# Kernel optimization log

Hardware: AMD Instinct MI355X
Metric: run time of the kernel (lower is better)

## Reference

```python
import jax, jax.numpy as jnp
import numpy as np

S = 41          # seq_len
D_IN = 1280
D_OUT = 1024
HEADS = 4
HC = D_OUT // HEADS
EPS = 1e-5

# ---- static edge construction (faithful to the torch code, incl. duplicate edges) ----

def _local_edges(s, window=1):
    e = []
    for i in range(s):
        for j in range(max(0, i - window), min(s, i + window + 1)):
            if i != j:
                e += [(i, j), (j, i)]
    return np.array(e, dtype=np.int32).T

def _region_edges(s):
    e = []
    step = s // 3
    for st in range(0, s, step):
        blk = range(st, min(st + step, s))
        for i in blk:
            for j in blk:
                if i != j:
                    e += [(i, j), (j, i)]
    return np.array(e, dtype=np.int32).T

def _global_edges(s):
    r, c = np.triu_indices(s, 1)  # torch.combinations: (i, j) with i < j
    return np.stack([r, c]).astype(np.int32)

def _batch_edges(e, b, s):
    off = np.arange(b, dtype=np.int32) * s
    return (e[:, None, :] + off[None, :, None]).reshape(2, -1)

_LOCAL = _local_edges(S)
_REGION = _region_edges(S)
_GLOBAL = _global_edges(S)

# ---- layer primitives ----

def _layernorm(x, g, b):
    mu = x.mean(-1, keepdims=True)
    v = ((x - mu) ** 2).mean(-1, keepdims=True)
    return (x - mu) / jnp.sqrt(v + EPS) * g + b

def _gcn(x, w, b, src, tgt, n):
    # PyG GCNConv: x' = D^-1/2 (A + I) D^-1/2 (x W) + b
    h = x @ w
    sl = jnp.arange(n, dtype=src.dtype)
    s = jnp.concatenate([src, sl]); t = jnp.concatenate([tgt, sl])
    deg = jax.ops.segment_sum(jnp.ones(t.shape, h.dtype), t, n)
    dinv = jnp.where(deg > 0, jax.lax.rsqrt(jnp.maximum(deg, 1.0)), 0.0)
    norm = dinv[s] * dinv[t]
    return jax.ops.segment_sum(h[s] * norm[:, None], t, n) + b

def _gat(x, w, a_src, a_dst, b, src, tgt, n):
    # PyG GATConv (shared lin, self loops, leaky_relu 0.2, softmax over incoming edges)
    h = (x @ w).reshape(n, HEADS, HC)
    sl = jnp.arange(n, dtype=src.dtype)
    s = jnp.concatenate([src, sl]); t = jnp.concatenate([tgt, sl])
    al_s = (h * a_src).sum(-1)  # [n, H]
    al_d = (h * a_dst).sum(-1)
    e = jax.nn.leaky_relu(al_s[s] + al_d[t], 0.2)  # [E, H]
    m = jax.ops.segment_max(e, t, n)
    ex = jnp.exp(e - m[t])
    den = jax.ops.segment_sum(ex, t, n)
    alpha = ex / den[t]
    out = jax.ops.segment_sum(h[s] * alpha[:, :, None], t, n)
    return out.reshape(n, HEADS * HC) + b

def _sage(x, wl, bl, wr, src, tgt, n):
    # PyG SAGEConv: mean-aggregate neighbors, plus root transform
    cnt = jax.ops.segment_sum(jnp.ones(src.shape, x.dtype), tgt, n)
    agg = jax.ops.segment_sum(x[src], tgt, n) / jnp.maximum(cnt, 1.0)[:, None]
    return agg @ wl + bl + x @ wr


def setup_inputs() -> dict:
    key = jax.random.key(0)
    ks = jax.random.split(key, 16)
    sc = 0.02
    f32 = jnp.float32
    inp = {
        'x': jax.random.normal(ks[0], (512, S, D_IN), f32),
        'att_w': jax.random.normal(ks[1], (D_IN, 1), f32) * sc,
        'att_b': jnp.zeros((1,), f32),
        'gcn_w': jax.random.normal(ks[2], (D_IN, D_OUT), f32) * sc,
        'gcn_b': jnp.zeros((D_OUT,), f32),
        'sn_g': jnp.ones((D_OUT,), f32), 'sn_b': jnp.zeros((D_OUT,), f32),
        'gat_w': jax.random.normal(ks[3], (D_IN, D_OUT), f32) * sc,
        'gat_as': jax.random.normal(ks[4], (HEADS, HC), f32) * sc,
        'gat_ad': jax.random.normal(ks[5], (HEADS, HC), f32) * sc,
        'gat_b': jnp.zeros((D_OUT,), f32),
        'mn_g': jnp.ones((D_OUT,), f32), 'mn_b': jnp.zeros((D_OUT,), f32),
        'sage_wl': jax.random.normal(ks[6], (D_IN, D_OUT), f32) * sc,
        'sage_bl': jnp.zeros((D_OUT,), f32),
        'sage_wr': jax.random.normal(ks[7], (D_IN, D_OUT), f32) * sc,
        'fp_w1': jax.random.normal(ks[8], (D_IN, 512), f32) * sc,
        'fp_b1': jnp.zeros((512,), f32),
        'fp_w2': jax.random.normal(ks[9], (512, S), f32) * sc,
        'fp_b2': jnp.zeros((S,), f32),
        'dn_g': jnp.ones((D_OUT,), f32), 'dn_b': jnp.zeros((D_OUT,), f32),
        'gate_w': jax.random.normal(ks[10], (3 * D_OUT, 3), f32) * sc,
        'gate_b': jnp.zeros((3,), f32),
    }
    return inp


def reference(x, att_w, att_b, gcn_w, gcn_b, sn_g, sn_b, gat_w, gat_as, gat_ad, gat_b,
              mn_g, mn_b, sage_wl, sage_bl, sage_wr, fp_w1, fp_b1, fp_w2, fp_b2,
              dn_g, dn_b, gate_w, gate_b):
    B = x.shape[0]
    N = B * S
    le = jnp.asarray(_batch_edges(_LOCAL, B, S))
    re = jnp.asarray(_batch_edges(_REGION, B, S))
    ge = jnp.asarray(_batch_edges(_GLOBAL, B, S))

    xf = x.reshape(N, D_IN)
    # shallow: local gating -> GCN -> LN
    enhanced = xf * jax.nn.sigmoid(xf @ att_w + att_b)
    shallow = _gcn(enhanced, gcn_w, gcn_b, le[0], le[1], N)
    shallow = _layernorm(shallow.reshape(B, S, D_OUT), sn_g, sn_b)
    # medium: GAT over region blocks -> LN
    gat = _gat(xf, gat_w, gat_as[None], gat_ad[None], gat_b, re[0], re[1], N)
    gat = _layernorm(gat.reshape(B, S, D_OUT), mn_g, mn_b)
    # deep: learned propagation mixing, SAGE over global edges -> LN
    pw = jax.nn.softmax(jax.nn.relu(x @ fp_w1 + fp_b1) @ fp_w2 + fp_b2, axis=-1)  # [B,S,S]
    sage_in = jnp.einsum('bij,bjd->bid', pw, x).reshape(N, D_IN)
    sage = _sage(sage_in, sage_wl, sage_bl, sage_wr, ge[0], ge[1], N)
    sage = _layernorm(sage.reshape(B, S, D_OUT), dn_g, dn_b)
    # gated branch mixing
    combined = jnp.concatenate([shallow, gat, sage], axis=-1)
    gates = jax.nn.softmax(combined @ gate_w + gate_b, axis=-1)
    total = gates[..., 0:1] * shallow + gates[..., 1:2] * gat + gates[..., 2:3] * sage
    return (shallow, gat, total)
```

## Files before the change

kernel.cpp:

```cpp
#include <hip/hip_runtime.h>
#include <math.h>

static constexpr int S    = 41;
static constexpr int DIN  = 1280;
static constexpr int DOUT = 1024;
static constexpr int HEADS = 4;
static constexpr int HC   = 256;

typedef __attribute__((ext_vector_type(4))) float f32x4;
typedef __attribute__((ext_vector_type(8))) short short8;

__device__ __forceinline__ ushort f2bf(float f) {
  uint u = __float_as_uint(f);
  uint r = u + 0x7fffu + ((u >> 16) & 1u);
  return (ushort)(r >> 16);
}
__device__ __forceinline__ float bf2f(ushort u) {
  return __uint_as_float(((uint)u) << 16);
}

__device__ __forceinline__ void gload16(const ushort* g, ushort* l) {
  __builtin_amdgcn_global_load_lds((const __attribute__((address_space(1))) void*)g,
                                   (__attribute__((address_space(3))) void*)l, 16, 0, 0);
}


__device__ __forceinline__ float warpReduceSum(float v) {
#pragma unroll
  for (int off = 32; off; off >>= 1) v += __shfl_down(v, off);
  return v;
}

__device__ __forceinline__ void blockReduce2(float& a, float& b) {
  a = warpReduceSum(a);
  b = warpReduceSum(b);
  __shared__ float red[8];
  int w = threadIdx.x >> 6, lane = threadIdx.x & 63;
  if (lane == 0) { red[w] = a; red[4 + w] = b; }
  __syncthreads();
  a = red[0] + red[1] + red[2] + red[3];
  b = red[4] + red[5] + red[6] + red[7];
}

__device__ __forceinline__ void blockReduce3(float& a, float& b, float& c) {
  a = warpReduceSum(a);
  b = warpReduceSum(b);
  c = warpReduceSum(c);
  __shared__ float red3[12];
  int w = threadIdx.x >> 6, lane = threadIdx.x & 63;
  if (lane == 0) { red3[w] = a; red3[4 + w] = b; red3[8 + w] = c; }
  __syncthreads();
  a = red3[0] + red3[1] + red3[2] + red3[3];
  b = red3[4] + red3[5] + red3[6] + red3[7];
  c = red3[8] + red3[9] + red3[10] + red3[11];
}


__global__ __launch_bounds__(256) void cvtsig_kernel(
    const float4* __restrict__ x, const float* __restrict__ att_w,
    const float* __restrict__ att_b, ushort4* __restrict__ xb, float* __restrict__ sig)
{
  int row  = blockIdx.x * 4 + (threadIdx.x >> 6);
  int lane = threadIdx.x & 63;
  const float4* xr = x + (size_t)row * (DIN / 4);
  const float4* wr = (const float4*)att_w;
  ushort4* xo = xb + (size_t)row * (DIN / 4);
  float acc = 0.f;
#pragma unroll
  for (int k = 0; k < DIN / 4 / 64; ++k) {
    float4 a = xr[lane + k * 64];
    float4 w = wr[lane + k * 64];
    acc += a.x * w.x + a.y * w.y + a.z * w.z + a.w * w.w;
    ushort4 o;
    o.x = f2bf(a.x); o.y = f2bf(a.y); o.z = f2bf(a.z); o.w = f2bf(a.w);
    xo[lane + k * 64] = o;
  }
  acc = warpReduceSum(acc);
  if (lane == 0) sig[row] = 1.f / (1.f + expf(-(acc + att_b[0])));
}


__global__ __launch_bounds__(256) void wcvt_kernel(const float* __restrict__ W,
                                                   ushort* __restrict__ out,
                                                   int K, int N, int ostride, int koff) {
  __shared__ float t[32][33];
  int n0 = blockIdx.x * 32, k0 = blockIdx.y * 32;
  int tx = threadIdx.x & 31, ty = threadIdx.x >> 5;
#pragma unroll
  for (int r = 0; r < 4; ++r) {
    int k = ty + r * 8;
    t[k][tx] = W[(size_t)(k0 + k) * N + n0 + tx];
  }
  __syncthreads();
#pragma unroll
  for (int r = 0; r < 4; ++r) {
    int nn = ty + r * 8;
    out[(size_t)(n0 + nn) * ostride + koff + k0 + tx] = f2bf(t[tx][nn]);
  }
}

__global__ __launch_bounds__(256) void w2cvt_kernel(const float* __restrict__ w2,
                                                    ushort* __restrict__ wpw) {
  int idx = blockIdx.x * 256 + threadIdx.x;
  int n = idx >> 9, k = idx & 511;
  wpw[idx] = (n < S) ? f2bf(w2[(size_t)k * S + n]) : (ushort)0;
}


struct Epi {
  void* dst0; void* dst1; void* dst2;
  const float* bias0; const float* bias1; const float* bias2;
  const float* rs0;
  int n1, n2;
  int ld0, ld1, ld2;
  int relu2;
};

template<bool F32OUT>
__global__ __launch_bounds__(256) void gemm_bf16(
    const ushort* __restrict__ A, const ushort* __restrict__ Bt, int K, Epi e)
{
  __shared__ __align__(16) ushort As[128 * 32];
  __shared__ __align__(16) ushort Bs[128 * 32];

  const int tid  = threadIdx.x;
  const int w    = tid >> 6;
  const int lane = tid & 63;
  const int l16  = lane & 15;
  const int l4   = lane >> 4;
  const int bm   = blockIdx.y * 128;
  const int bn   = blockIdx.x * 128;
  const int m0   = (w >> 1) * 64;
  const int n0   = (w & 1) * 64;

  const int srow = w * 32 + (lane >> 2);
  const int scol = (lane & 3) * 8;

  f32x4 acc[4][4];
#pragma unroll
  for (int i = 0; i < 4; ++i)
#pragma unroll
    for (int j = 0; j < 4; ++j) acc[i][j] = (f32x4)0.f;

  const ushort* pA0 = A  + (size_t)(bm + srow) * K + scol;
  const ushort* pA1 = A  + (size_t)(bm + srow + 16) * K + scol;
  const ushort* pB0 = Bt + (size_t)(bn + srow) * K + scol;
  const ushort* pB1 = Bt + (size_t)(bn + srow + 16) * K + scol;
  ushort* lA0 = &As[w * 1024];
  ushort* lA1 = &As[w * 1024 + 512];
  ushort* lB0 = &Bs[w * 1024];
  ushort* lB1 = &Bs[w * 1024 + 512];

  for (int kt = 0; kt < K; kt += 32) {
    gload16(pA0 + kt, lA0);
    gload16(pA1 + kt, lA1);
    gload16(pB0 + kt, lB0);
    gload16(pB1 + kt, lB1);
    __syncthreads();

    short8 a[4], b[4];
#pragma unroll
    for (int i = 0; i < 4; ++i)
      a[i] = *reinterpret_cast<const short8*>(&As[(m0 + i * 16 + l16) * 32 + l4 * 8]);
#pragma unroll
    for (int j = 0; j < 4; ++j)
      b[j] = *reinterpret_cast<const short8*>(&Bs[(n0 + j * 16 + l16) * 32 + l4 * 8]);
#pragma unroll
    for (int i = 0; i < 4; ++i)
#pragma unroll
      for (int j = 0; j < 4; ++j)
        acc[i][j] = __builtin_amdgcn_mfma_f32_16x16x32_bf16(a[i], b[j], acc[i][j], 0, 0, 0);
    __syncthreads();
  }

  void* dstv; const float* bias; const float* rs = nullptr; int ldc, cb, relu = 0;
  if (bn < e.n1)      { dstv = e.dst0; ldc = e.ld0; cb = bn;        bias = e.bias0; rs = e.rs0; }
  else if (bn < e.n2) { dstv = e.dst1; ldc = e.ld1; cb = bn - e.n1; bias = e.bias1; }
  else                { dstv = e.dst2; ldc = e.ld2; cb = bn - e.n2; bias = e.bias2; relu = e.relu2; }

#pragma unroll
  for (int i = 0; i < 4; ++i) {
    int mbase = bm + m0 + i * 16 + l4 * 4;
    float rsv[4];
#pragma unroll
    for (int r = 0; r < 4; ++r) rsv[r] = rs ? rs[mbase + r] : 1.f;
#pragma unroll
    for (int j = 0; j < 4; ++j) {
      int col = cb + n0 + j * 16 + l16;
      float bv = bias ? bias[col] : 0.f;
#pragma unroll
      for (int r = 0; r < 4; ++r) {
        float t = acc[i][j][r] * rsv[r] + bv;
        if (relu) t = fmaxf(t, 0.f);
        if (F32OUT) ((float*)dstv)[(size_t)(mbase + r) * ldc + col] = t;
        else        ((ushort*)dstv)[(size_t)(mbase + r) * ldc + col] = f2bf(t);
      }
    }
  }
}


__device__ __forceinline__ float dinv_local(int j) {
  return rsqrtf((j == 0 || j == S - 1) ? 3.f : 5.f);
}

__global__ __launch_bounds__(256) void gcnln_kernel(
    const ushort* __restrict__ h, const float* __restrict__ gcn_b,
    const float* __restrict__ g, const float* __restrict__ be, float* __restrict__ out)
{
  int n = blockIdx.x;
  int i = n % S;
  int tid = threadIdx.x;
  int d0 = tid * 4;
  float di = dinv_local(i);
  float wc = di * di;
  float wl = (i > 0)     ? 2.f * di * dinv_local(i - 1) : 0.f;
  float wr = (i < S - 1) ? 2.f * di * dinv_local(i + 1) : 0.f;
  const ushort* hc = h + (size_t)n * DOUT + d0;
  ushort4 c4 = *(const ushort4*)hc;
  ushort4 lft = (i > 0)     ? *(const ushort4*)(hc - DOUT) : ushort4{0, 0, 0, 0};
  ushort4 rgt = (i < S - 1) ? *(const ushort4*)(hc + DOUT) : ushort4{0, 0, 0, 0};
  float4 b4 = *(const float4*)(gcn_b + d0);
  float vals[4];
  const ushort* cp = (const ushort*)&c4;
  const ushort* lp = (const ushort*)&lft;
  const ushort* rp = (const ushort*)&rgt;
  const float* bp = (const float*)&b4;
  float s = 0.f, sq = 0.f;
#pragma unroll
  for (int q = 0; q < 4; ++q) {
    float v = wc * bf2f(cp[q]) + wl * bf2f(lp[q]) + wr * bf2f(rp[q]) + bp[q];
    vals[q] = v;
    s += v; sq += v * v;
  }
  blockReduce2(s, sq);
  float mu = s * (1.f / DOUT);
  float var = sq * (1.f / DOUT) - mu * mu;
  float rstd = rsqrtf(var + 1e-5f);
  float4 g4 = *(const float4*)(g + d0);
  float4 e4 = *(const float4*)(be + d0);
  const float* gp = (const float*)&g4;
  const float* ep = (const float*)&e4;
  float4 o4;
  float* op = (float*)&o4;
#pragma unroll
  for (int q = 0; q < 4; ++q) op[q] = (vals[q] - mu) * rstd * gp[q] + ep[q];
  *(float4*)(out + (size_t)n * DOUT + d0) = o4;
}


__global__ __launch_bounds__(256) void gat_fused(
    const ushort* __restrict__ h, const float* __restrict__ as_,
    const float* __restrict__ ad_, const float* __restrict__ gat_b,
    const float* __restrict__ g, const float* __restrict__ be,
    float* __restrict__ out)
{
  int b  = blockIdx.x >> 2;
  int rb = blockIdx.x & 3;
  int lo = rb * 13;
  int cnt = (rb < 3) ? 13 : 2;
  __shared__ __align__(16) ushort hs[13][DOUT];
  __shared__ float alpha[13][13][HEADS];
  __shared__ float als_l[13][HEADS], ald_l[13][HEADS];
  int tid = threadIdx.x;
  int wv = tid >> 6, lane = tid & 63;

  for (int r = 0; r < cnt; ++r) {
    const ushort4* src = (const ushort4*)(h + (size_t)(b * S + lo + r) * DOUT);
    ((ushort4*)hs[r])[tid] = src[tid];
  }
  __syncthreads();

  {
    const float4* a4 = (const float4*)(as_ + wv * HC);
    const float4* d4 = (const float4*)(ad_ + wv * HC);
    float4 av = a4[lane], dv = d4[lane];
    for (int s = 0; s < cnt; ++s) {
      ushort4 hv4 = ((const ushort4*)&hs[s][wv * HC])[lane];
      float h0 = bf2f(hv4.x), h1 = bf2f(hv4.y), h2 = bf2f(hv4.z), h3 = bf2f(hv4.w);
      float a = h0 * av.x + h1 * av.y + h2 * av.z + h3 * av.w;
      float d = h0 * dv.x + h1 * dv.y + h2 * dv.z + h3 * dv.w;
      a = warpReduceSum(a);
      d = warpReduceSum(d);
      if (lane == 0) { als_l[s][wv] = a; ald_l[s][wv] = d; }
    }
  }
  __syncthreads();

  if (tid < cnt * HEADS) {
    int t = tid >> 2, hd = tid & 3;
    float myald = ald_l[t][hd];
    float m = -1e30f;
    for (int s = 0; s < cnt; ++s) {
      float v = als_l[s][hd] + myald;
      v = (v > 0.f) ? v : 0.2f * v;
      m = fmaxf(m, v);
    }
    float den = 0.f;
    for (int s = 0; s < cnt; ++s) {
      float v = als_l[s][hd] + myald;
      v = (v > 0.f) ? v : 0.2f * v;
      float ev = expf(v - m) * ((s == t) ? 1.f : 2.f);
      alpha[t][s][hd] = ev;
      den += ev;
    }
    float inv = 1.f / den;
    for (int s = 0; s < cnt; ++s) alpha[t][s][hd] *= inv;
  }
  __syncthreads();

  float gbv[4], gv[4], ev[4];
#pragma unroll
  for (int q = 0; q < 4; ++q) {
    int d = q * 256 + tid;
    gbv[q] = gat_b[d]; gv[q] = g[d]; ev[q] = be[d];
  }
  for (int t = 0; t < cnt; ++t) {
    float vals[4];
    float s = 0.f, sq = 0.f;
#pragma unroll
    for (int q = 0; q < 4; ++q) {
      int d = q * 256 + tid;
      float accv = 0.f;
      for (int si = 0; si < cnt; ++si)
        accv += alpha[t][si][q] * bf2f(hs[si][d]);
      accv += gbv[q];
      vals[q] = accv;
      s += accv; sq += accv * accv;
    }
    blockReduce2(s, sq);
    float mu = s * (1.f / DOUT);
    float var = sq * (1.f / DOUT) - mu * mu;
    float rstd = rsqrtf(var + 1e-5f);
    float* o = out + (size_t)(b * S + lo + t) * DOUT;
#pragma unroll
    for (int q = 0; q < 4; ++q) {
      int d = q * 256 + tid;
      o[d] = (vals[q] - mu) * rstd * gv[q] + ev[q];
    }
    __syncthreads();
  }
}


__global__ __launch_bounds__(256) void sagein_kernel(
    const float* __restrict__ fp2, const float* __restrict__ fp_b2,
    const ushort* __restrict__ xb, ushort* __restrict__ sa)
{
  int b = blockIdx.y;
  int d0 = blockIdx.x * 256;
  int tid = threadIdx.x, wv = tid >> 6, lane = tid & 63;
  __shared__ float pws[S][S];
  for (int i = wv; i < S; i += 4) {
    float v = (lane < S) ? (fp2[(size_t)(b * S + i) * 128 + lane] + fp_b2[lane]) : -1e30f;
    float m = v;
#pragma unroll
    for (int off = 32; off; off >>= 1) m = fmaxf(m, __shfl_xor(m, off));
    float e = (lane < S) ? expf(v - m) : 0.f;
    float sum = e;
#pragma unroll
    for (int off = 32; off; off >>= 1) sum += __shfl_xor(sum, off);
    if (lane < S) pws[i][lane] = e / sum;
  }
  __syncthreads();
  float xreg[S];
  const ushort* xp = xb + (size_t)b * S * DIN + d0 + tid;
#pragma unroll
  for (int j = 0; j < S; ++j) xreg[j] = bf2f(xp[(size_t)j * DIN]);
  float prefix = 0.f;
  for (int i = 0; i < S; ++i) {
    float v = 0.f;
#pragma unroll
    for (int j = 0; j < S; ++j) v += pws[i][j] * xreg[j];
    size_t base = (size_t)(b * S + i) * (2 * DIN) + d0 + tid;
    sa[base] = f2bf(v);
    sa[base + DIN] = f2bf((i > 0) ? (prefix / (float)i) : 0.f);
    prefix += v;
  }
}


__global__ __launch_bounds__(256) void lngate_kernel(
    const ushort* __restrict__ hbuf, const float* __restrict__ dn_g,
    const float* __restrict__ dn_b, const float* __restrict__ gw,
    const float* __restrict__ gb, float* __restrict__ out, int N)
{
  size_t OUT = (size_t)N * DOUT;
  int n = blockIdx.x;
  int tid = threadIdx.x;
  int d0 = tid * 4;

  ushort4 h4 = *(const ushort4*)(hbuf + (size_t)n * DOUT + d0);
  const ushort* hp = (const ushort*)&h4;
  float hv[4];
  float s = 0.f, sq = 0.f;
#pragma unroll
  for (int q = 0; q < 4; ++q) {
    hv[q] = bf2f(hp[q]);
    s += hv[q]; sq += hv[q] * hv[q];
  }
  blockReduce2(s, sq);
  float mu = s * (1.f / DOUT);
  float var = sq * (1.f / DOUT) - mu * mu;
  float rstd = rsqrtf(var + 1e-5f);
  float4 g4 = *(const float4*)(dn_g + d0);
  float4 b4 = *(const float4*)(dn_b + d0);
  const float* gp = (const float*)&g4;
  const float* bp = (const float*)&b4;
  float sa_[4];
#pragma unroll
  for (int q = 0; q < 4; ++q) sa_[q] = (hv[q] - mu) * rstd * gp[q] + bp[q];

  float4 sh4 = *(const float4*)(out + (size_t)n * DOUT + d0);
  float4 ga4 = *(const float4*)(out + OUT + (size_t)n * DOUT + d0);
  const float* shp = (const float*)&sh4;
  const float* gap = (const float*)&ga4;

  float p0 = 0.f, p1 = 0.f, p2 = 0.f;
#pragma unroll
  for (int q = 0; q < 4; ++q) {
    int d = d0 + q;
    const float* w0 = gw + (size_t)d * 3;
    const float* w1 = gw + (size_t)(DOUT + d) * 3;
    const float* w2 = gw + (size_t)(2 * DOUT + d) * 3;
    p0 += shp[q] * w0[0] + gap[q] * w1[0] + sa_[q] * w2[0];
    p1 += shp[q] * w0[1] + gap[q] * w1[1] + sa_[q] * w2[1];
    p2 += shp[q] * w0[2] + gap[q] * w1[2] + sa_[q] * w2[2];
  }
  blockReduce3(p0, p1, p2);
  p0 += gb[0]; p1 += gb[1]; p2 += gb[2];
  float m = fmaxf(p0, fmaxf(p1, p2));
  float e0 = expf(p0 - m), e1 = expf(p1 - m), e2 = expf(p2 - m);
  float inv = 1.f / (e0 + e1 + e2);
  float g0 = e0 * inv, g1 = e1 * inv, g2 = e2 * inv;
  float4 o4;
  float* op = (float*)&o4;
#pragma unroll
  for (int q = 0; q < 4; ++q) op[q] = g0 * shp[q] + g1 * gap[q] + g2 * sa_[q];
  *(float4*)(out + 2 * OUT + (size_t)n * DOUT + d0) = o4;
}


extern "C" void kernel_launch(void* const* d_in, const int* in_sizes, int n_in,
                              void* d_out, int out_size, void* d_ws, size_t ws_size,
                              hipStream_t stream) {
  const float* x       = (const float*)d_in[0];
  const float* att_w   = (const float*)d_in[1];
  const float* att_b   = (const float*)d_in[2];
  const float* gcn_w   = (const float*)d_in[3];
  const float* gcn_b   = (const float*)d_in[4];
  const float* sn_g    = (const float*)d_in[5];
  const float* sn_b    = (const float*)d_in[6];
  const float* gat_w   = (const float*)d_in[7];
  const float* gat_as  = (const float*)d_in[8];
  const float* gat_ad  = (const float*)d_in[9];
  const float* gat_b   = (const float*)d_in[10];
  const float* mn_g    = (const float*)d_in[11];
  const float* mn_b    = (const float*)d_in[12];
  const float* sage_wl = (const float*)d_in[13];
  const float* sage_bl = (const float*)d_in[14];
  const float* sage_wr = (const float*)d_in[15];
  const float* fp_w1   = (const float*)d_in[16];
  const float* fp_b1   = (const float*)d_in[17];
  const float* fp_w2   = (const float*)d_in[18];
  const float* fp_b2   = (const float*)d_in[19];
  const float* dn_g    = (const float*)d_in[20];
  const float* dn_b    = (const float*)d_in[21];
  const float* gate_w  = (const float*)d_in[22];
  const float* gate_b  = (const float*)d_in[23];

  const int B = in_sizes[0] / (S * DIN);
  const int N = B * S;
  float* out = (float*)d_out;

  char* ws = (char*)d_ws;
  size_t off = 0;
  auto alloc = [&](size_t bytes) { size_t p = off; off += (bytes + 255) & ~(size_t)255; return p; };
  ushort* xb   = (ushort*)(ws + alloc((size_t)N * DIN * 2));
  ushort* Bt1  = (ushort*)(ws + alloc((size_t)2560 * DIN * 2));
  ushort* Bt2  = (ushort*)(ws + alloc((size_t)DOUT * 2 * DIN * 2));
  ushort* wpw  = (ushort*)(ws + alloc((size_t)128 * 512 * 2));
  ushort* gcnh = (ushort*)(ws + alloc((size_t)N * DOUT * 2));
  ushort* Cgat = (ushort*)(ws + alloc((size_t)N * DOUT * 2));
  ushort* fp1  = (ushort*)(ws + alloc((size_t)N * 512 * 2));
  ushort* sa   = (ushort*)(ws + alloc((size_t)N * 2 * DIN * 2));
  float*  sig  = (float*)(ws + alloc((size_t)N * 4));
  float*  fp2  = (float*)Cgat;
  ushort* hbuf = gcnh;

  dim3 blk(256);

  cvtsig_kernel<<<N / 4, blk, 0, stream>>>((const float4*)x, att_w, att_b, (ushort4*)xb, sig);
  wcvt_kernel<<<dim3(DOUT / 32, DIN / 32), blk, 0, stream>>>(gcn_w, Bt1, DIN, DOUT, DIN, 0);
  wcvt_kernel<<<dim3(DOUT / 32, DIN / 32), blk, 0, stream>>>(gat_w, Bt1 + (size_t)1024 * DIN, DIN, DOUT, DIN, 0);
  wcvt_kernel<<<dim3(512 / 32, DIN / 32), blk, 0, stream>>>(fp_w1, Bt1 + (size_t)2048 * DIN, DIN, 512, DIN, 0);
  wcvt_kernel<<<dim3(DOUT / 32, DIN / 32), blk, 0, stream>>>(sage_wr, Bt2, DIN, DOUT, 2 * DIN, 0);
  wcvt_kernel<<<dim3(DOUT / 32, DIN / 32), blk, 0, stream>>>(sage_wl, Bt2, DIN, DOUT, 2 * DIN, DIN);
  w2cvt_kernel<<<dim3(128 * 512 / 256), blk, 0, stream>>>(fp_w2, wpw);

  Epi e1;
  e1.dst0 = gcnh; e1.dst1 = Cgat; e1.dst2 = fp1;
  e1.bias0 = nullptr; e1.bias1 = nullptr; e1.bias2 = fp_b1;
  e1.rs0 = sig;
  e1.n1 = 1024; e1.n2 = 2048;
  e1.ld0 = DOUT; e1.ld1 = DOUT; e1.ld2 = 512;
  e1.relu2 = 1;
  gemm_bf16<false><<<dim3(2560 / 128, N / 128), blk, 0, stream>>>(xb, Bt1, DIN, e1);

  gcnln_kernel<<<N, blk, 0, stream>>>(gcnh, gcn_b, sn_g, sn_b, out);

  gat_fused<<<B * 4, blk, 0, stream>>>(Cgat, gat_as, gat_ad, gat_b, mn_g, mn_b,
                                       out + (size_t)N * DOUT);

  Epi epw;
  epw.dst0 = fp2; epw.dst1 = nullptr; epw.dst2 = nullptr;
  epw.bias0 = nullptr; epw.bias1 = nullptr; epw.bias2 = nullptr;
  epw.rs0 = nullptr;
  epw.n1 = 1 << 30; epw.n2 = 1 << 30;
  epw.ld0 = 128; epw.ld1 = 128; epw.ld2 = 128;
  epw.relu2 = 0;
  gemm_bf16<true><<<dim3(1, N / 128), blk, 0, stream>>>(fp1, wpw, 512, epw);

  sagein_kernel<<<dim3(DIN / 256, B), blk, 0, stream>>>(fp2, fp_b2, xb, sa);

  Epi e2;
  e2.dst0 = hbuf; e2.dst1 = nullptr; e2.dst2 = nullptr;
  e2.bias0 = sage_bl; e2.bias1 = nullptr; e2.bias2 = nullptr;
  e2.rs0 = nullptr;
  e2.n1 = 1 << 30; e2.n2 = 1 << 30;
  e2.ld0 = DOUT; e2.ld1 = DOUT; e2.ld2 = DOUT;
  e2.relu2 = 0;
  gemm_bf16<false><<<dim3(DOUT / 128, N / 128), blk, 0, stream>>>(sa, Bt2, 2 * DIN, e2);

  lngate_kernel<<<N, blk, 0, stream>>>(hbuf, dn_g, dn_b, gate_w, gate_b, out, N);
}
```

Measured before the change: 764.8 us.

## Reassociate SAGE propagation: project x first, then mix in output space

Uses linearity to apply the SAGE weight matrices to x before the learned propagation mixing. Both projections (Wr and Wl) are appended to the first fused GEMM, so a single larger GEMM over all five weight slices replaces the separate SAGE GEMM that used K=2*DIN. The mixing kernel then applies the softmax propagation weights and their prefix-mean to the projected features in the 1024-wide output space and adds the bias. The GEMM grid is also flattened to 1D with an XCD-aware block remap. The change removes a dependent GEMM and the wide intermediate sa buffer. In exchange the mix kernel holds two 41-element register arrays, and bf16 rounding now happens at a different point, so numerics shift slightly.

```diff
diff --git a/kernel.cpp b/kernel.cpp
--- a/kernel.cpp
+++ b/kernel.cpp
@@ -108,28 +108,36 @@
 
 
 struct Epi {
-  void* dst0; void* dst1; void* dst2;
-  const float* bias0; const float* bias1; const float* bias2;
-  const float* rs0;
-  int n1, n2;
-  int ld0, ld1, ld2;
-  int relu2;
+  void* dst[5];
+  const float* bias[5];
+  int nend[5];
+  int ld[5];
+  int relu[5];
+  const float* rs;
 };
 
 template<bool F32OUT>
 __global__ __launch_bounds__(256) void gemm_bf16(
-    const ushort* __restrict__ A, const ushort* __restrict__ Bt, int K, Epi e)
+    const ushort* __restrict__ A, const ushort* __restrict__ Bt, int K, int nb, Epi e)
 {
   __shared__ __align__(16) ushort As[128 * 32];
   __shared__ __align__(16) ushort Bs[128 * 32];
+
+  int bid = blockIdx.x;
+  int nwg = gridDim.x;
+  int wg = bid;
+  if ((nwg & 7) == 0) {
+    int cpx = nwg >> 3;
+    wg = (bid & 7) * cpx + (bid >> 3);
+  }
+  const int bn = (wg % nb) * 128;
+  const int bm = (wg / nb) * 128;
 
   const int tid  = threadIdx.x;
   const int w    = tid >> 6;
   const int lane = tid & 63;
   const int l16  = lane & 15;
   const int l4   = lane >> 4;
-  const int bm   = blockIdx.y * 128;
-  const int bn   = blockIdx.x * 128;
   const int m0   = (w >> 1) * 64;
   const int n0   = (w & 1) * 64;
 
@@ -173,10 +181,12 @@
     __syncthreads();
   }
 
-  void* dstv; const float* bias; const float* rs = nullptr; int ldc, cb, relu = 0;
-  if (bn < e.n1)      { dstv = e.dst0; ldc = e.ld0; cb = bn;        bias = e.bias0; rs = e.rs0; }
-  else if (bn < e.n2) { dstv = e.dst1; ldc = e.ld1; cb = bn - e.n1; bias = e.bias1; }
-  else                { dstv = e.dst2; ldc = e.ld2; cb = bn - e.n2; bias = e.bias2; relu = e.relu2; }
+  void* dstv; const float* bias; const float* rs = nullptr; int ldc, cb, relu;
+  if (bn < e.nend[0])      { dstv = e.dst[0]; ldc = e.ld[0]; cb = bn;             bias = e.bias[0]; relu = e.relu[0]; rs = e.rs; }
+  else if (bn < e.nend[1]) { dstv = e.dst[1]; ldc = e.ld[1]; cb = bn - e.nend[0]; bias = e.bias[1]; relu = e.relu[1]; }
+  else if (bn < e.nend[2]) { dstv = e.dst[2]; ldc = e.ld[2]; cb = bn - e.nend[1]; bias = e.bias[2]; relu = e.relu[2]; }
+  else if (bn < e.nend[3]) { dstv = e.dst[3]; ldc = e.ld[3]; cb = bn - e.nend[2]; bias = e.bias[3]; relu = e.relu[3]; }
+  else                     { dstv = e.dst[4]; ldc = e.ld[4]; cb = bn - e.nend[3]; bias = e.bias[4]; relu = e.relu[4]; }
 
 #pragma unroll
   for (int i = 0; i < 4; ++i) {
@@ -343,14 +353,17 @@
 }
 
 
-__global__ __launch_bounds__(256) void sagein_kernel(
+__global__ __launch_bounds__(256) void mix_kernel(
     const float* __restrict__ fp2, const float* __restrict__ fp_b2,
-    const ushort* __restrict__ xb, ushort* __restrict__ sa)
+    const ushort* __restrict__ xr, const ushort* __restrict__ xl,
+    const float* __restrict__ sage_bl, ushort* __restrict__ hbuf)
 {
-  int b = blockIdx.y;
+  int b  = blockIdx.y;
   int d0 = blockIdx.x * 256;
   int tid = threadIdx.x, wv = tid >> 6, lane = tid & 63;
   __shared__ float pws[S][S];
+  __shared__ float cpw[S][S];
+
   for (int i = wv; i < S; i += 4) {
     float v = (lane < S) ? (fp2[(size_t)(b * S + i) * 128 + lane] + fp_b2[lane]) : -1e30f;
     float m = v;
@@ -363,19 +376,32 @@
     if (lane < S) pws[i][lane] = e / sum;
   }
   __syncthreads();
-  float xreg[S];
-  const ushort* xp = xb + (size_t)b * S * DIN + d0 + tid;
-#pragma unroll
-  for (int j = 0; j < S; ++j) xreg[j] = bf2f(xp[(size_t)j * DIN]);
-  float prefix = 0.f;
+
+  if (tid < S) {
+    float run = 0.f;
+    for (int i = 0; i < S; ++i) {
+      cpw[i][tid] = (i > 0) ? run / (float)i : 0.f;
+      run += pws[i][tid];
+    }
+  }
+  __syncthreads();
+
+  float xrv[S], xlv[S];
+  const ushort* xrp = xr + (size_t)(b * S) * DOUT + d0 + tid;
+  const ushort* xlp = xl + (size_t)(b * S) * DOUT + d0 + tid;
+#pragma unroll
+  for (int j = 0; j < S; ++j) {
+    xrv[j] = bf2f(xrp[(size_t)j * DOUT]);
+    xlv[j] = bf2f(xlp[(size_t)j * DOUT]);
+  }
+  float bl = sage_bl[d0 + tid];
+  ushort* op = hbuf + (size_t)(b * S) * DOUT + d0 + tid;
   for (int i = 0; i < S; ++i) {
-    float v = 0.f;
-#pragma unroll
-    for (int j = 0; j < S; ++j) v += pws[i][j] * xreg[j];
-    size_t base = (size_t)(b * S + i) * (2 * DIN) + d0 + tid;
-    sa[base] = f2bf(v);
-    sa[base + DIN] = f2bf((i > 0) ? (prefix / (float)i) : 0.f);
-    prefix += v;
+    float acc = bl;
+#pragma unroll
+    for (int j = 0; j < S; ++j)
+      acc += pws[i][j] * xrv[j] + cpw[i][j] * xlv[j];
+    op[(size_t)i * DOUT] = f2bf(acc);
   }
 }
 
@@ -471,19 +497,20 @@
 
   const int B = in_sizes[0] / (S * DIN);
   const int N = B * S;
+  const int NMEGA = 4608;
   float* out = (float*)d_out;
 
   char* ws = (char*)d_ws;
   size_t off = 0;
   auto alloc = [&](size_t bytes) { size_t p = off; off += (bytes + 255) & ~(size_t)255; return p; };
   ushort* xb   = (ushort*)(ws + alloc((size_t)N * DIN * 2));
-  ushort* Bt1  = (ushort*)(ws + alloc((size_t)2560 * DIN * 2));
-  ushort* Bt2  = (ushort*)(ws + alloc((size_t)DOUT * 2 * DIN * 2));
+  ushort* Bt   = (ushort*)(ws + alloc((size_t)NMEGA * DIN * 2));
   ushort* wpw  = (ushort*)(ws + alloc((size_t)128 * 512 * 2));
   ushort* gcnh = (ushort*)(ws + alloc((size_t)N * DOUT * 2));
   ushort* Cgat = (ushort*)(ws + alloc((size_t)N * DOUT * 2));
   ushort* fp1  = (ushort*)(ws + alloc((size_t)N * 512 * 2));
-  ushort* sa   = (ushort*)(ws + alloc((size_t)N * 2 * DIN * 2));
+  ushort* xr   = (ushort*)(ws + alloc((size_t)N * DOUT * 2));
+  ushort* xl   = (ushort*)(ws + alloc((size_t)N * DOUT * 2));
   float*  sig  = (float*)(ws + alloc((size_t)N * 4));
   float*  fp2  = (float*)Cgat;
   ushort* hbuf = gcnh;
@@ -491,21 +518,21 @@
   dim3 blk(256);
 
   cvtsig_kernel<<<N / 4, blk, 0, stream>>>((const float4*)x, att_w, att_b, (ushort4*)xb, sig);
-  wcvt_kernel<<<dim3(DOUT / 32, DIN / 32), blk, 0, stream>>>(gcn_w, Bt1, DIN, DOUT, DIN, 0);
-  wcvt_kernel<<<dim3(DOUT / 32, DIN / 32), blk, 0, stream>>>(gat_w, Bt1 + (size_t)1024 * DIN, DIN, DOUT, DIN, 0);
-  wcvt_kernel<<<dim3(512 / 32, DIN / 32), blk, 0, stream>>>(fp_w1, Bt1 + (size_t)2048 * DIN, DIN, 512, DIN, 0);
-  wcvt_kernel<<<dim3(DOUT / 32, DIN / 32), blk, 0, stream>>>(sage_wr, Bt2, DIN, DOUT, 2 * DIN, 0);
-  wcvt_kernel<<<dim3(DOUT / 32, DIN / 32), blk, 0, stream>>>(sage_wl, Bt2, DIN, DOUT, 2 * DIN, DIN);
+  wcvt_kernel<<<dim3(DOUT / 32, DIN / 32), blk, 0, stream>>>(gcn_w, Bt, DIN, DOUT, DIN, 0);
+  wcvt_kernel<<<dim3(DOUT / 32, DIN / 32), blk, 0, stream>>>(gat_w, Bt + (size_t)1024 * DIN, DIN, DOUT, DIN, 0);
+  wcvt_kernel<<<dim3(512 / 32, DIN / 32), blk, 0, stream>>>(fp_w1, Bt + (size_t)2048 * DIN, DIN, 512, DIN, 0);
+  wcvt_kernel<<<dim3(DOUT / 32, DIN / 32), blk, 0, stream>>>(sage_wr, Bt + (size_t)2560 * DIN, DIN, DOUT, DIN, 0);
+  wcvt_kernel<<<dim3(DOUT / 32, DIN / 32), blk, 0, stream>>>(sage_wl, Bt + (size_t)3584 * DIN, DIN, DOUT, DIN, 0);
   w2cvt_kernel<<<dim3(128 * 512 / 256), blk, 0, stream>>>(fp_w2, wpw);
 
   Epi e1;
-  e1.dst0 = gcnh; e1.dst1 = Cgat; e1.dst2 = fp1;
-  e1.bias0 = nullptr; e1.bias1 = nullptr; e1.bias2 = fp_b1;
-  e1.rs0 = sig;
-  e1.n1 = 1024; e1.n2 = 2048;
-  e1.ld0 = DOUT; e1.ld1 = DOUT; e1.ld2 = 512;
-  e1.relu2 = 1;
-  gemm_bf16<false><<<dim3(2560 / 128, N / 128), blk, 0, stream>>>(xb, Bt1, DIN, e1);
+  e1.dst[0] = gcnh; e1.dst[1] = Cgat; e1.dst[2] = fp1; e1.dst[3] = xr; e1.dst[4] = xl;
+  e1.bias[0] = nullptr; e1.bias[1] = nullptr; e1.bias[2] = fp_b1; e1.bias[3] = nullptr; e1.bias[4] = nullptr;
+  e1.nend[0] = 1024; e1.nend[1] = 2048; e1.nend[2] = 2560; e1.nend[3] = 3584; e1.nend[4] = 4608;
+  e1.ld[0] = DOUT; e1.ld[1] = DOUT; e1.ld[2] = 512; e1.ld[3] = DOUT; e1.ld[4] = DOUT;
+  e1.relu[0] = 0; e1.relu[1] = 0; e1.relu[2] = 1; e1.relu[3] = 0; e1.relu[4] = 0;
+  e1.rs = sig;
+  gemm_bf16<false><<<dim3((NMEGA / 128) * (N / 128)), blk, 0, stream>>>(xb, Bt, DIN, NMEGA / 128, e1);
 
   gcnln_kernel<<<N, blk, 0, stream>>>(gcnh, gcn_b, sn_g, sn_b, out);
 
@@ -513,24 +540,15 @@
                                        out + (size_t)N * DOUT);
 
   Epi epw;
-  epw.dst0 = fp2; epw.dst1 = nullptr; epw.dst2 = nullptr;
-  epw.bias0 = nullptr; epw.bias1 = nullptr; epw.bias2 = nullptr;
-  epw.rs0 = nullptr;
-  epw.n1 = 1 << 30; epw.n2 = 1 << 30;
-  epw.ld0 = 128; epw.ld1 = 128; epw.ld2 = 128;
-  epw.relu2 = 0;
-  gemm_bf16<true><<<dim3(1, N / 128), blk, 0, stream>>>(fp1, wpw, 512, epw);
-
-  sagein_kernel<<<dim3(DIN / 256, B), blk, 0, stream>>>(fp2, fp_b2, xb, sa);
-
-  Epi e2;
-  e2.dst0 = hbuf; e2.dst1 = nullptr; e2.dst2 = nullptr;
-  e2.bias0 = sage_bl; e2.bias1 = nullptr; e2.bias2 = nullptr;
-  e2.rs0 = nullptr;
-  e2.n1 = 1 << 30; e2.n2 = 1 << 30;
-  e2.ld0 = DOUT; e2.ld1 = DOUT; e2.ld2 = DOUT;
-  e2.relu2 = 0;
-  gemm_bf16<false><<<dim3(DOUT / 128, N / 128), blk, 0, stream>>>(sa, Bt2, 2 * DIN, e2);
+  epw.dst[0] = fp2; epw.dst[1] = nullptr; epw.dst[2] = nullptr; epw.dst[3] = nullptr; epw.dst[4] = nullptr;
+  epw.bias[0] = nullptr; epw.bias[1] = nullptr; epw.bias[2] = nullptr; epw.bias[3] = nullptr; epw.bias[4] = nullptr;
+  epw.nend[0] = 1 << 30; epw.nend[1] = 1 << 30; epw.nend[2] = 1 << 30; epw.nend[3] = 1 << 30; epw.nend[4] = 1 << 30;
+  epw.ld[0] = 128; epw.ld[1] = 128; epw.ld[2] = 128; epw.ld[3] = 128; epw.ld[4] = 128;
+  epw.relu[0] = 0; epw.relu[1] = 0; epw.relu[2] = 0; epw.relu[3] = 0; epw.relu[4] = 0;
+  epw.rs = nullptr;
+  gemm_bf16<true><<<dim3(N / 128), blk, 0, stream>>>(fp1, wpw, 512, 1, epw);
+
+  mix_kernel<<<dim3(DOUT / 256, B), blk, 0, stream>>>(fp2, fp_b2, xr, xl, sage_bl, hbuf);
 
   lngate_kernel<<<N, blk, 0, stream>>>(hbuf, dn_g, dn_b, gate_w, gate_b, out, N);
 }
```

New measurement: 837.1 us. 9.5% more time.
